# Kernel optimization log

Hardware: AMD Instinct MI355X
Metric: run time of the kernel (lower is better)

Reference implementation:

```python
import jax, jax.numpy as jnp
import numpy as np

N = 8192       # nodes
E = 262144     # edges (avg degree 32)
IN_DIM, HID, EMB = 512, 256, 64


def setup_inputs() -> dict:
    key = jax.random.key(0)
    ks = jax.random.split(key, 7)
    features = jax.random.normal(ks[0], (N, IN_DIM), dtype=jnp.float32)
    edge_index = jax.random.randint(ks[1], (2, E), 0, N, dtype=jnp.int32)
    edge_weight = jax.random.uniform(ks[2], (E,), dtype=jnp.float32)
    W0 = jax.random.normal(ks[3], (IN_DIM, HID), dtype=jnp.float32) * (1.0 / np.sqrt(IN_DIM))
    W_mean = jax.random.normal(ks[4], (HID, EMB), dtype=jnp.float32) * (1.0 / np.sqrt(HID))
    W_logstd = jax.random.normal(ks[5], (HID, EMB), dtype=jnp.float32) * (1.0 / np.sqrt(HID))
    noise = jax.random.normal(ks[6], (N, EMB), dtype=jnp.float32)
    return {"features": features, "edge_index": edge_index, "edge_weight": edge_weight,
            "W0": W0, "W_mean": W_mean, "W_logstd": W_logstd, "noise": noise}


def reference(features, edge_index, edge_weight, W0, W_mean, W_logstd, noise):
    src, dst = edge_index[0], edge_index[1]
    n = features.shape[0]

    def gcn(x, W):
        h = x @ W                                   # dense transform first (smaller dim)
        msg = h[src] * edge_weight[:, None]         # gather + weight
        return jax.ops.segment_sum(msg, dst, num_segments=n)  # scatter-add aggregate

    hidden = gcn(features, W0)                       # [N, HID] (gcn_base, no activation)
    mean = jax.nn.relu(gcn(hidden, W_mean))          # [N, EMB]
    logstd = jax.nn.relu(gcn(hidden, W_logstd))      # [N, EMB]
    Z = noise * jnp.exp(logstd) + mean               # reparameterization
    adj_logits = Z @ Z.T                             # [N, N] inner-product decoder
    return adj_logits
```

## Files before the change

### kernel.cpp

```cpp
#include <hip/hip_runtime.h>
#include <hip/hip_bf16.h>

#define N_NODES 8192
#define N_EDGES 262144
#define IN_DIM  512
#define HID     256
#define EMB     64
#define C2      128

__global__ __launch_bounds__(256) void k_count(const int* __restrict__ dst, int* __restrict__ deg) {
    int e = blockIdx.x * 256 + threadIdx.x;
    atomicAdd(&deg[dst[e]], 1);
}

__global__ __launch_bounds__(1024) void k_scan(const int* __restrict__ deg, int* __restrict__ rowptr) {
    __shared__ int part[1024];
    const int t = threadIdx.x;
    const int base = t * 8;
    int v[8], incl[8];
    int s = 0;
    #pragma unroll
    for (int j = 0; j < 8; ++j) { v[j] = deg[base + j]; s += v[j]; incl[j] = s; }
    part[t] = s;
    __syncthreads();
    for (int off = 1; off < 1024; off <<= 1) {
        int x = (t >= off) ? part[t - off] : 0;
        __syncthreads();
        part[t] += x;
        __syncthreads();
    }
    int excl = part[t] - s;
    if (t == 0) rowptr[0] = 0;
    #pragma unroll
    for (int j = 0; j < 8; ++j) rowptr[base + j + 1] = excl + incl[j];
}

__global__ __launch_bounds__(256) void k_fill(const int* __restrict__ src, const int* __restrict__ dst,
                                              const float* __restrict__ ew, const int* __restrict__ rowptr,
                                              int* __restrict__ cursor, int* __restrict__ srcs,
                                              float* __restrict__ wsorted) {
    int e = blockIdx.x * 256 + threadIdx.x;
    int d = dst[e];
    int p = rowptr[d] + atomicAdd(&cursor[d], 1);
    srcs[p] = src[e];
    wsorted[p] = ew[e];
}

__global__ __launch_bounds__(256) void k_wc(const float* __restrict__ W0, const float* __restrict__ Wm,
                                            const float* __restrict__ Wl, float* __restrict__ WcT) {
    __shared__ float w0s[16][256];
    const int t = threadIdx.x;
    const int kb = blockIdx.x * 16;
    #pragma unroll
    for (int m = 0; m < 4; ++m) {
        int f = t + 256 * m;
        int row = f >> 6, q = f & 63;
        *(float4*)&w0s[row][q * 4] = *(const float4*)&W0[(size_t)(kb + row) * 256 + q * 4];
    }
    __syncthreads();
    const int j = t & 127, kh = t >> 7;
    const float* B = (j < 64) ? (Wm + j) : (Wl + (j - 64));
    float acc[8] = {};
    for (int h = 0; h < 256; h += 4) {
        float b0 = B[(h + 0) * 64], b1 = B[(h + 1) * 64];
        float b2 = B[(h + 2) * 64], b3 = B[(h + 3) * 64];
        #pragma unroll
        for (int r = 0; r < 8; ++r) {
            float4 x = *(const float4*)&w0s[kh * 8 + r][h];
            acc[r] += x.x * b0 + x.y * b1 + x.z * b2 + x.w * b3;
        }
    }
    #pragma unroll
    for (int r = 0; r < 8; ++r)
        WcT[(size_t)j * 512 + kb + kh * 8 + r] = acc[r];
}

__global__ __launch_bounds__(256) void k_gemm_p(const float* __restrict__ X, const float* __restrict__ WcT,
                                                float* __restrict__ P) {
    __shared__ float Xs[32][68];
    const int t = threadIdx.x;
    const int i0 = blockIdx.x * 32;
    const int rg = t >> 6, cpair = t & 63, c0 = cpair * 2;
    float acc[8][2] = {};
    for (int kc = 0; kc < 512; kc += 64) {
        #pragma unroll
        for (int m = 0; m < 2; ++m) {
            int f = t + 256 * m;
            int row = f >> 4, q = f & 15;
            *(float4*)&Xs[row][q * 4] = *(const float4*)&X[(size_t)(i0 + row) * 512 + kc + q * 4];
        }
        __syncthreads();
        #pragma unroll 4
        for (int k4 = 0; k4 < 16; ++k4) {
            float4 wA = *(const float4*)&WcT[(size_t)c0 * 512 + kc + k4 * 4];
            float4 wB = *(const float4*)&WcT[(size_t)(c0 + 1) * 512 + kc + k4 * 4];
            #pragma unroll
            for (int r = 0; r < 8; ++r) {
                float4 x = *(const float4*)&Xs[rg * 8 + r][k4 * 4];
                acc[r][0] += x.x * wA.x + x.y * wA.y + x.z * wA.z + x.w * wA.w;
                acc[r][1] += x.x * wB.x + x.y * wB.y + x.z * wB.z + x.w * wB.w;
            }
        }
        __syncthreads();
    }
    #pragma unroll
    for (int r = 0; r < 8; ++r) {
        float2 v = make_float2(acc[r][0], acc[r][1]);
        *(float2*)&P[(size_t)(i0 + rg * 8 + r) * 128 + c0] = v;
    }
}

__global__ __launch_bounds__(128) void k_agg(const float* __restrict__ In, const int* __restrict__ rowptr,
                                             const int* __restrict__ srcs, const float* __restrict__ wsorted,
                                             float* __restrict__ Out, const float* __restrict__ noise,
                                             float* __restrict__ Z, int zpass) {
    const int b = blockIdx.x, t = threadIdx.x;
    const int beg = rowptr[b], end = rowptr[b + 1];
    float a0 = 0.f, a1 = 0.f, a2 = 0.f, a3 = 0.f;
    int i = beg;
    for (; i + 4 <= end; i += 4) {
        int   s0 = srcs[i],     s1 = srcs[i + 1], s2 = srcs[i + 2], s3 = srcs[i + 3];
        float w0 = wsorted[i],  w1 = wsorted[i + 1], w2 = wsorted[i + 2], w3 = wsorted[i + 3];
        a0 += In[(size_t)s0 * C2 + t] * w0;
        a1 += In[(size_t)s1 * C2 + t] * w1;
        a2 += In[(size_t)s2 * C2 + t] * w2;
        a3 += In[(size_t)s3 * C2 + t] * w3;
    }
    for (; i < end; ++i)
        a0 += In[(size_t)srcs[i] * C2 + t] * wsorted[i];
    float acc = (a0 + a1) + (a2 + a3);
    if (!zpass) {
        Out[(size_t)b * C2 + t] = acc;
    } else {
        __shared__ float u[C2];
        u[t] = acc;
        __syncthreads();
        if (t < 64) {
            float m = fmaxf(u[t], 0.f);
            float l = fmaxf(u[t + 64], 0.f);
            float z = noise[(size_t)b * 64 + t] * expf(fminf(l, 80.f)) + m;
            z = fminf(fmaxf(z, -1e18f), 1e18f);
            Z[(size_t)b * 64 + t] = z;
        }
    }
}

__global__ __launch_bounds__(256) void k_zzt(const float* __restrict__ Z, float* __restrict__ out) {
    if (blockIdx.x < blockIdx.y) return;
    __shared__ float S[128][64];
    const int t = threadIdx.x;
    const int tx = t & 15, ty = t >> 4;
    const int i0 = blockIdx.y * 128, j0 = blockIdx.x * 128;
    #pragma unroll
    for (int m = 0; m < 8; ++m) {
        int f = t + 256 * m;
        int row = f >> 4, q = f & 15;
        float4 v = *(const float4*)&Z[(size_t)(j0 + row) * 64 + q * 4];
        *(float4*)&S[row][(q * 4) ^ ((row >> 3 & 7) << 2)] = v;
    }
    const float* A0 = Z + (size_t)(i0 + ty * 4) * 64;
    const float* A1 = Z + (size_t)(i0 + 64 + ty * 4) * 64;
    const int rb0 = tx * 4, rb1 = 64 + tx * 4;
    const int swz = ((tx >> 1) & 7) << 2;
    __syncthreads();
    float acc[2][4][2][4] = {};
    for (int k = 0; k < 64; k += 4) {
        const int ks = k ^ swz;
        float4 a[2][4], b[2][4];
        #pragma unroll
        for (int r = 0; r < 4; ++r) {
            a[0][r] = *(const float4*)&A0[r * 64 + k];
            a[1][r] = *(const float4*)&A1[r * 64 + k];
            b[0][r] = *(const float4*)&S[rb0 + r][ks];
            b[1][r] = *(const float4*)&S[rb1 + r][ks];
        }
        #pragma unroll
        for (int rg = 0; rg < 2; ++rg)
            #pragma unroll
            for (int r = 0; r < 4; ++r)
                #pragma unroll
                for (int cg = 0; cg < 2; ++cg)
                    #pragma unroll
                    for (int c = 0; c < 4; ++c)
                        acc[rg][r][cg][c] += a[rg][r].x * b[cg][c].x + a[rg][r].y * b[cg][c].y
                                           + a[rg][r].z * b[cg][c].z + a[rg][r].w * b[cg][c].w;
    }
    #pragma unroll
    for (int rg = 0; rg < 2; ++rg)
        #pragma unroll
        for (int r = 0; r < 4; ++r) {
            size_t row = (size_t)(i0 + rg * 64 + ty * 4 + r);
            #pragma unroll
            for (int cg = 0; cg < 2; ++cg) {
                float4 v = make_float4(acc[rg][r][cg][0], acc[rg][r][cg][1],
                                       acc[rg][r][cg][2], acc[rg][r][cg][3]);
                *(float4*)&out[row * N_NODES + j0 + cg * 64 + tx * 4] = v;
            }
        }
    if (i0 != j0) {
        #pragma unroll
        for (int cg = 0; cg < 2; ++cg)
            #pragma unroll
            for (int c = 0; c < 4; ++c) {
                size_t row = (size_t)(j0 + cg * 64 + tx * 4 + c);
                #pragma unroll
                for (int rg = 0; rg < 2; ++rg) {
                    float4 v = make_float4(acc[rg][0][cg][c], acc[rg][1][cg][c],
                                           acc[rg][2][cg][c], acc[rg][3][cg][c]);
                    *(float4*)&out[row * N_NODES + i0 + rg * 64 + ty * 4] = v;
                }
            }
    }
}

extern "C" void kernel_launch(void* const* d_in, const int* in_sizes, int n_in,
                              void* d_out, int out_size, void* d_ws, size_t ws_size,
                              hipStream_t stream) {
    const float* X     = (const float*)d_in[0];
    const int*   ei    = (const int*)d_in[1];
    const float* ew    = (const float*)d_in[2];
    const float* W0    = (const float*)d_in[3];
    const float* Wm    = (const float*)d_in[4];
    const float* Wl    = (const float*)d_in[5];
    const float* noise = (const float*)d_in[6];
    float* out = (float*)d_out;

    const int* srcI = ei;
    const int* dstI = ei + N_EDGES;

    int*   deg     = (int*)d_ws;
    int*   cursor  = deg + 8192;
    int*   rowptr  = deg + 16384;
    int*   srcs    = deg + 24592;
    float* wsorted = (float*)(deg + 24592 + N_EDGES);
    float* WcT     = wsorted + N_EDGES;
    float* P       = WcT + 128 * 512;
    float* U1      = P + (size_t)N_NODES * C2;
    float* Z       = U1 + (size_t)N_NODES * C2;

    hipMemsetAsync(deg, 0, 16384 * sizeof(int), stream);

    k_count<<<N_EDGES / 256, 256, 0, stream>>>(dstI, deg);
    k_scan<<<1, 1024, 0, stream>>>(deg, rowptr);
    k_fill<<<N_EDGES / 256, 256, 0, stream>>>(srcI, dstI, ew, rowptr, cursor, srcs, wsorted);
    k_wc<<<32, 256, 0, stream>>>(W0, Wm, Wl, WcT);
    k_gemm_p<<<N_NODES / 32, 256, 0, stream>>>(X, WcT, P);
    k_agg<<<N_NODES, 128, 0, stream>>>(P, rowptr, srcs, wsorted, U1, nullptr, nullptr, 0);
    k_agg<<<N_NODES, 128, 0, stream>>>(U1, rowptr, srcs, wsorted, nullptr, noise, Z, 1);
    k_zzt<<<dim3(N_NODES / 128, N_NODES / 128), 256, 0, stream>>>(Z, out);
}
```

Baseline: 522.0 us.

## Merge setup kernels and stage mirrored ZZ^T tile stores through shared memory

The degree count is merged with the weight-product kernel, and the prefix scan is merged with the feature GEMM, so independent work shares a launch and the pipeline drops from eight launches to six. The scan now runs in 256 threads with 32 elements each and vectorized loads. In the symmetric Z·Zᵀ kernel, the transposed mirror tile is first written into a padded shared buffer and then stored as coalesced full-row float4 writes, replacing strided column writes. The cost is extra shared-memory traffic, two more barriers per half tile, and a single scan block that may finish after the GEMM blocks.

After: 475.1 us. 9.0% less time.

```diff
diff --git a/kernel.cpp b/kernel.cpp
--- a/kernel.cpp
+++ b/kernel.cpp
@@ -8,22 +8,93 @@
 #define EMB     64
 #define C2      128
 
-__global__ __launch_bounds__(256) void k_count(const int* __restrict__ dst, int* __restrict__ deg) {
-    int e = blockIdx.x * 256 + threadIdx.x;
-    atomicAdd(&deg[dst[e]], 1);
-}
-
-__global__ __launch_bounds__(1024) void k_scan(const int* __restrict__ deg, int* __restrict__ rowptr) {
-    __shared__ int part[1024];
+__global__ __launch_bounds__(256) void k_count_wc(const int* __restrict__ dst, int* __restrict__ deg,
+                                                  const float* __restrict__ W0, const float* __restrict__ Wm,
+                                                  const float* __restrict__ Wl, float* __restrict__ WcT) {
+    __shared__ float w0s[16][256];
     const int t = threadIdx.x;
-    const int base = t * 8;
-    int v[8], incl[8];
+    if (blockIdx.x < 1024) {
+        int e = blockIdx.x * 256 + t;
+        atomicAdd(&deg[dst[e]], 1);
+        return;
+    }
+    const int kb = (blockIdx.x - 1024) * 16;
+    #pragma unroll
+    for (int m = 0; m < 4; ++m) {
+        int f = t + 256 * m;
+        int row = f >> 6, q = f & 63;
+        *(float4*)&w0s[row][q * 4] = *(const float4*)&W0[(size_t)(kb + row) * 256 + q * 4];
+    }
+    __syncthreads();
+    const int j = t & 127, kh = t >> 7;
+    const float* B = (j < 64) ? (Wm + j) : (Wl + (j - 64));
+    float acc[8] = {};
+    for (int h = 0; h < 256; h += 4) {
+        float b0 = B[(h + 0) * 64], b1 = B[(h + 1) * 64];
+        float b2 = B[(h + 2) * 64], b3 = B[(h + 3) * 64];
+        #pragma unroll
+        for (int r = 0; r < 8; ++r) {
+            float4 x = *(const float4*)&w0s[kh * 8 + r][h];
+            acc[r] += x.x * b0 + x.y * b1 + x.z * b2 + x.w * b3;
+        }
+    }
+    #pragma unroll
+    for (int r = 0; r < 8; ++r)
+        WcT[(size_t)j * 512 + kb + kh * 8 + r] = acc[r];
+}
+
+__global__ __launch_bounds__(256) void k_scan_gemm(const int* __restrict__ deg, int* __restrict__ rowptr,
+                                                   const float* __restrict__ X, const float* __restrict__ WcT,
+                                                   float* __restrict__ P) {
+    const int t = threadIdx.x;
+    if (blockIdx.x < 256) {
+        __shared__ float Xs[32][68];
+        const int i0 = blockIdx.x * 32;
+        const int rg = t >> 6, cpair = t & 63, c0 = cpair * 2;
+        float acc[8][2] = {};
+        for (int kc = 0; kc < 512; kc += 64) {
+            #pragma unroll
+            for (int m = 0; m < 2; ++m) {
+                int f = t + 256 * m;
+                int row = f >> 4, q = f & 15;
+                *(float4*)&Xs[row][q * 4] = *(const float4*)&X[(size_t)(i0 + row) * 512 + kc + q * 4];
+            }
+            __syncthreads();
+            #pragma unroll 4
+            for (int k4 = 0; k4 < 16; ++k4) {
+                float4 wA = *(const float4*)&WcT[(size_t)c0 * 512 + kc + k4 * 4];
+                float4 wB = *(const float4*)&WcT[(size_t)(c0 + 1) * 512 + kc + k4 * 4];
+                #pragma unroll
+                for (int r = 0; r < 8; ++r) {
+                    float4 x = *(const float4*)&Xs[rg * 8 + r][k4 * 4];
+                    acc[r][0] += x.x * wA.x + x.y * wA.y + x.z * wA.z + x.w * wA.w;
+                    acc[r][1] += x.x * wB.x + x.y * wB.y + x.z * wB.z + x.w * wB.w;
+                }
+            }
+            __syncthreads();
+        }
+        #pragma unroll
+        for (int r = 0; r < 8; ++r) {
+            float2 v = make_float2(acc[r][0], acc[r][1]);
+            *(float2*)&P[(size_t)(i0 + rg * 8 + r) * 128 + c0] = v;
+        }
+        return;
+    }
+    __shared__ int part[256];
+    const int base = t * 32;
+    int incl[32];
     int s = 0;
     #pragma unroll
-    for (int j = 0; j < 8; ++j) { v[j] = deg[base + j]; s += v[j]; incl[j] = s; }
+    for (int j4 = 0; j4 < 8; ++j4) {
+        int4 d = *(const int4*)&deg[base + j4 * 4];
+        s += d.x; incl[j4 * 4 + 0] = s;
+        s += d.y; incl[j4 * 4 + 1] = s;
+        s += d.z; incl[j4 * 4 + 2] = s;
+        s += d.w; incl[j4 * 4 + 3] = s;
+    }
     part[t] = s;
     __syncthreads();
-    for (int off = 1; off < 1024; off <<= 1) {
+    for (int off = 1; off < 256; off <<= 1) {
         int x = (t >= off) ? part[t - off] : 0;
         __syncthreads();
         part[t] += x;
@@ -32,7 +103,7 @@
     int excl = part[t] - s;
     if (t == 0) rowptr[0] = 0;
     #pragma unroll
-    for (int j = 0; j < 8; ++j) rowptr[base + j + 1] = excl + incl[j];
+    for (int j = 0; j < 32; ++j) rowptr[base + j + 1] = excl + incl[j];
 }
 
 __global__ __launch_bounds__(256) void k_fill(const int* __restrict__ src, const int* __restrict__ dst,
@@ -44,70 +115,6 @@
     int p = rowptr[d] + atomicAdd(&cursor[d], 1);
     srcs[p] = src[e];
     wsorted[p] = ew[e];
-}
-
-__global__ __launch_bounds__(256) void k_wc(const float* __restrict__ W0, const float* __restrict__ Wm,
-                                            const float* __restrict__ Wl, float* __restrict__ WcT) {
-    __shared__ float w0s[16][256];
-    const int t = threadIdx.x;
-    const int kb = blockIdx.x * 16;
-    #pragma unroll
-    for (int m = 0; m < 4; ++m) {
-        int f = t + 256 * m;
-        int row = f >> 6, q = f & 63;
-        *(float4*)&w0s[row][q * 4] = *(const float4*)&W0[(size_t)(kb + row) * 256 + q * 4];
-    }
-    __syncthreads();
-    const int j = t & 127, kh = t >> 7;
-    const float* B = (j < 64) ? (Wm + j) : (Wl + (j - 64));
-    float acc[8] = {};
-    for (int h = 0; h < 256; h += 4) {
-        float b0 = B[(h + 0) * 64], b1 = B[(h + 1) * 64];
-        float b2 = B[(h + 2) * 64], b3 = B[(h + 3) * 64];
-        #pragma unroll
-        for (int r = 0; r < 8; ++r) {
-            float4 x = *(const float4*)&w0s[kh * 8 + r][h];
-            acc[r] += x.x * b0 + x.y * b1 + x.z * b2 + x.w * b3;
-        }
-    }
-    #pragma unroll
-    for (int r = 0; r < 8; ++r)
-        WcT[(size_t)j * 512 + kb + kh * 8 + r] = acc[r];
-}
-
-__global__ __launch_bounds__(256) void k_gemm_p(const float* __restrict__ X, const float* __restrict__ WcT,
-                                                float* __restrict__ P) {
-    __shared__ float Xs[32][68];
-    const int t = threadIdx.x;
-    const int i0 = blockIdx.x * 32;
-    const int rg = t >> 6, cpair = t & 63, c0 = cpair * 2;
-    float acc[8][2] = {};
-    for (int kc = 0; kc < 512; kc += 64) {
-        #pragma unroll
-        for (int m = 0; m < 2; ++m) {
-            int f = t + 256 * m;
-            int row = f >> 4, q = f & 15;
-            *(float4*)&Xs[row][q * 4] = *(const float4*)&X[(size_t)(i0 + row) * 512 + kc + q * 4];
-        }
-        __syncthreads();
-        #pragma unroll 4
-        for (int k4 = 0; k4 < 16; ++k4) {
-            float4 wA = *(const float4*)&WcT[(size_t)c0 * 512 + kc + k4 * 4];
-            float4 wB = *(const float4*)&WcT[(size_t)(c0 + 1) * 512 + kc + k4 * 4];
-            #pragma unroll
-            for (int r = 0; r < 8; ++r) {
-                float4 x = *(const float4*)&Xs[rg * 8 + r][k4 * 4];
-                acc[r][0] += x.x * wA.x + x.y * wA.y + x.z * wA.z + x.w * wA.w;
-                acc[r][1] += x.x * wB.x + x.y * wB.y + x.z * wB.z + x.w * wB.w;
-            }
-        }
-        __syncthreads();
-    }
-    #pragma unroll
-    for (int r = 0; r < 8; ++r) {
-        float2 v = make_float2(acc[r][0], acc[r][1]);
-        *(float2*)&P[(size_t)(i0 + rg * 8 + r) * 128 + c0] = v;
-    }
 }
 
 __global__ __launch_bounds__(128) void k_agg(const float* __restrict__ In, const int* __restrict__ rowptr,
@@ -147,7 +154,7 @@
 
 __global__ __launch_bounds__(256) void k_zzt(const float* __restrict__ Z, float* __restrict__ out) {
     if (blockIdx.x < blockIdx.y) return;
-    __shared__ float S[128][64];
+    __shared__ float S[8448];
     const int t = threadIdx.x;
     const int tx = t & 15, ty = t >> 4;
     const int i0 = blockIdx.y * 128, j0 = blockIdx.x * 128;
@@ -156,7 +163,7 @@
         int f = t + 256 * m;
         int row = f >> 4, q = f & 15;
         float4 v = *(const float4*)&Z[(size_t)(j0 + row) * 64 + q * 4];
-        *(float4*)&S[row][(q * 4) ^ ((row >> 3 & 7) << 2)] = v;
+        *(float4*)&S[row * 64 + ((q * 4) ^ ((row >> 3 & 7) << 2))] = v;
     }
     const float* A0 = Z + (size_t)(i0 + ty * 4) * 64;
     const float* A1 = Z + (size_t)(i0 + 64 + ty * 4) * 64;
@@ -171,8 +178,8 @@
         for (int r = 0; r < 4; ++r) {
             a[0][r] = *(const float4*)&A0[r * 64 + k];
             a[1][r] = *(const float4*)&A1[r * 64 + k];
-            b[0][r] = *(const float4*)&S[rb0 + r][ks];
-            b[1][r] = *(const float4*)&S[rb1 + r][ks];
+            b[0][r] = *(const float4*)&S[(rb0 + r) * 64 + ks];
+            b[1][r] = *(const float4*)&S[(rb1 + r) * 64 + ks];
         }
         #pragma unroll
         for (int rg = 0; rg < 2; ++rg)
@@ -199,17 +206,27 @@
         }
     if (i0 != j0) {
         #pragma unroll
-        for (int cg = 0; cg < 2; ++cg)
+        for (int cg = 0; cg < 2; ++cg) {
+            __syncthreads();
             #pragma unroll
             for (int c = 0; c < 4; ++c) {
-                size_t row = (size_t)(j0 + cg * 64 + tx * 4 + c);
+                int col = tx * 4 + c;
                 #pragma unroll
                 for (int rg = 0; rg < 2; ++rg) {
                     float4 v = make_float4(acc[rg][0][cg][c], acc[rg][1][cg][c],
                                            acc[rg][2][cg][c], acc[rg][3][cg][c]);
-                    *(float4*)&out[row * N_NODES + i0 + rg * 64 + ty * 4] = v;
+                    *(float4*)&S[col * 132 + rg * 64 + ty * 4] = v;
                 }
             }
+            __syncthreads();
+            #pragma unroll
+            for (int m = 0; m < 8; ++m) {
+                int f = t + 256 * m;
+                int row = f >> 5, q = f & 31;
+                float4 v = *(const float4*)&S[row * 132 + q * 4];
+                *(float4*)&out[(size_t)(j0 + cg * 64 + row) * N_NODES + i0 + q * 4] = v;
+            }
+        }
     }
 }
 
@@ -240,11 +257,9 @@
 
     hipMemsetAsync(deg, 0, 16384 * sizeof(int), stream);
 
-    k_count<<<N_EDGES / 256, 256, 0, stream>>>(dstI, deg);
-    k_scan<<<1, 1024, 0, stream>>>(deg, rowptr);
+    k_count_wc<<<1024 + 32, 256, 0, stream>>>(dstI, deg, W0, Wm, Wl, WcT);
+    k_scan_gemm<<<256 + 1, 256, 0, stream>>>(deg, rowptr, X, WcT, P);
     k_fill<<<N_EDGES / 256, 256, 0, stream>>>(srcI, dstI, ew, rowptr, cursor, srcs, wsorted);
-    k_wc<<<32, 256, 0, stream>>>(W0, Wm, Wl, WcT);
-    k_gemm_p<<<N_NODES / 32, 256, 0, stream>>>(X, WcT, P);
     k_agg<<<N_NODES, 128, 0, stream>>>(P, rowptr, srcs, wsorted, U1, nullptr, nullptr, 0);
     k_agg<<<N_NODES, 128, 0, stream>>>(U1, rowptr, srcs, wsorted, nullptr, noise, Z, 1);
     k_zzt<<<dim3(N_NODES / 128, N_NODES / 128), 256, 0, stream>>>(Z, out);
```
